# Optimization experiments

Hardware: AMD Instinct MI355X
Metric: run time of the kernel (lower is better)

Reference implementation:

```python
import jax, jax.numpy as jnp
import numpy as np

D_MODEL = 768
NUM_HEADS = 12
D_HEAD = D_MODEL // NUM_HEADS


def setup_inputs() -> dict:
    key = jax.random.key(0)
    ks = jax.random.split(key, 12)
    B, S = 2, 2048
    s = 1.0 / np.sqrt(D_MODEL)
    inp = {
        "query": jax.random.normal(ks[0], (B, S, D_MODEL), dtype=jnp.float32),
        "key": jax.random.normal(ks[1], (B, S, D_MODEL), dtype=jnp.float32),
        "value": jax.random.normal(ks[2], (B, S, D_MODEL), dtype=jnp.float32),
        "mask": jax.random.randint(ks[3], (B, 1, 1, S), 0, 2, dtype=jnp.int32),
        "Wq": jax.random.normal(ks[4], (D_MODEL, D_MODEL), dtype=jnp.float32) * s,
        "bq": jnp.zeros((D_MODEL,), dtype=jnp.float32),
        "Wk": jax.random.normal(ks[5], (D_MODEL, D_MODEL), dtype=jnp.float32) * s,
        "bk": jnp.zeros((D_MODEL,), dtype=jnp.float32),
        "Wv": jax.random.normal(ks[6], (D_MODEL, D_MODEL), dtype=jnp.float32) * s,
        "bv": jnp.zeros((D_MODEL,), dtype=jnp.float32),
        "Wo": jax.random.normal(ks[7], (D_MODEL, D_MODEL), dtype=jnp.float32) * s,
        "bo": jnp.zeros((D_MODEL,), dtype=jnp.float32),
    }
    return inp


def _split_heads(x):
    # [B, S, D] -> [B, H, S, Dh]
    B, S, _ = x.shape
    return x.reshape(B, S, NUM_HEADS, D_HEAD).transpose(0, 2, 1, 3)


def reference(query, key, value, mask, Wq, bq, Wk, bk, Wv, bv, Wo, bo):
    q = _split_heads(query @ Wq + bq)
    k = _split_heads(key @ Wk + bk)
    v = _split_heads(value @ Wv + bv)
    scores = jnp.einsum("bhqd,bhkd->bhqk", q, k) / jnp.sqrt(jnp.float32(D_HEAD))
    scores = jnp.where(mask == 0, -jnp.inf, scores)
    attn = jax.nn.softmax(scores, axis=-1)  # dropout is identity at inference
    ctx = jnp.einsum("bhqk,bhkd->bhqd", attn, v)
    B, _, S, _ = ctx.shape
    ctx = ctx.transpose(0, 2, 1, 3).reshape(B, S, D_MODEL)
    return ctx @ Wo + bo
```

## Files before the change

kernel.cpp:

```cpp
#include <hip/hip_runtime.h>
#include <stdint.h>

#define D_MODEL 768
#define SEQ     2048
#define BATCH   2
#define NHEAD   12
#define DHEAD   64
#define MROWS   (BATCH * SEQ)

typedef __bf16 bf16x8 __attribute__((ext_vector_type(8)));
typedef float  f32x4  __attribute__((ext_vector_type(4)));
typedef unsigned short u16;
typedef u16 u16x4 __attribute__((ext_vector_type(4)));
typedef uint32_t u32;

__device__ __forceinline__ u16 f32_to_bf16(float x) {
    u32 u = __float_as_uint(x);
    u32 r = (u + 0x7FFFu + ((u >> 16) & 1u)) >> 16;
    return (u16)r;
}
__device__ __forceinline__ float bf16_to_f32(u16 h) {
    return __uint_as_float(((u32)h) << 16);
}
__device__ __forceinline__ void split2(float x, u16 &hi, u16 &lo) {
    hi = f32_to_bf16(x);
    lo = f32_to_bf16(x - bf16_to_f32(hi));
}
__device__ __forceinline__ u32 pack2t(float a, float b) {
    return __builtin_amdgcn_perm(__float_as_uint(b), __float_as_uint(a), 0x07060302u);
}

__device__ __forceinline__ void stage16(const u16* g, const u16* l) {
    __builtin_amdgcn_global_load_lds(
        (const __attribute__((address_space(1))) u32*)g,
        (__attribute__((address_space(3))) u32*)l,
        16, 0, 0);
}

#define SRC_C8(lane)  ((((lane) & 3) ^ (((lane) >> 3) & 3)) * 8)
#define RD_C8(quad, l16) (((quad) ^ (((l16) >> 1) & 3)) * 8)

#define QSCALE 0.1803368801111204f
#define MSHIFT 20.0f

__global__ void prep_all(const float* __restrict__ q, const float* __restrict__ k,
                         const float* __restrict__ v, u16* __restrict__ xbase,
                         const float* __restrict__ Wq, const float* __restrict__ Wk,
                         const float* __restrict__ Wv, const float* __restrict__ Wo,
                         u16* __restrict__ wtbase,
                         const int* __restrict__ Mask, float* __restrict__ BiasM)
{
    __shared__ float tile[32][33];
    const int bx = blockIdx.x;
    if (bx < 9216) {
        const int t = bx / 3072;
        const float* src = (t == 0) ? q : (t == 1) ? k : v;
        const size_t P = (size_t)MROWS * D_MODEL;
        u16* xh = xbase + (size_t)t * 2 * P;
        u16* xl = xh + P;
        size_t idx = ((size_t)(bx % 3072) * 256 + threadIdx.x) * 4;
        float4 val = *reinterpret_cast<const float4*>(&src[idx]);
        float vv[4] = {val.x, val.y, val.z, val.w};
        u16x4 h4, l4;
        #pragma unroll
        for (int j = 0; j < 4; ++j) { u16 h, l; split2(vv[j], h, l); h4[j] = h; l4[j] = l; }
        *reinterpret_cast<u16x4*>(&xh[idx]) = h4;
        *reinterpret_cast<u16x4*>(&xl[idx]) = l4;
    } else if (bx < 11520) {
        int r = bx - 9216;
        int w = r / 576; r %= 576;
        int ky = r / 24, nx = r % 24;
        const float* W = (w == 0) ? Wq : (w == 1) ? Wk : (w == 2) ? Wv : Wo;
        const size_t WP = (size_t)D_MODEL * D_MODEL;
        u16* th = wtbase + (size_t)w * 2 * WP;
        u16* tl = th + WP;
        const int tx = threadIdx.x & 31, ty = threadIdx.x >> 5;
        const int n0 = nx * 32, k0 = ky * 32;
        #pragma unroll
        for (int rr = 0; rr < 4; ++rr) {
            int kk = k0 + ty + rr * 8;
            tile[ty + rr * 8][tx] = W[(size_t)kk * D_MODEL + n0 + tx];
        }
        __syncthreads();
        #pragma unroll
        for (int rr = 0; rr < 4; ++rr) {
            int n = n0 + ty + rr * 8;
            float val = tile[tx][ty + rr * 8];
            u16 h, l; split2(val, h, l);
            th[(size_t)n * D_MODEL + k0 + tx] = h;
            tl[(size_t)n * D_MODEL + k0 + tx] = l;
        }
    } else {
        int i = (bx - 11520) * 256 + threadIdx.x;
        BiasM[i] = (Mask[i] == 0) ? -3e38f : -MSHIFT;
    }
}

__global__ __launch_bounds__(256, 4) void gemm3(
    const u16* __restrict__ Ah0, const u16* __restrict__ Al0,
    const u16* __restrict__ Ah1, const u16* __restrict__ Al1,
    const u16* __restrict__ Ah2, const u16* __restrict__ Al2,
    const u16* __restrict__ Bh0, const u16* __restrict__ Bl0,
    const u16* __restrict__ Bh1, const u16* __restrict__ Bl1,
    const u16* __restrict__ Bh2, const u16* __restrict__ Bl2,
    const float* __restrict__ bias0, const float* __restrict__ bias1,
    const float* __restrict__ bias2,
    u16* __restrict__ Qhl, u16* __restrict__ Khl, u16* __restrict__ Vt,
    float* __restrict__ Out, int mode)
{
    const int z = (mode == 3) ? 3 : (int)blockIdx.z;
    const u16 *GAh, *GAl, *GBh, *GBl; const float* Bias;
    if (z == 1)      { GAh = Ah1; GAl = Al1; GBh = Bh1; GBl = Bl1; Bias = bias1; }
    else if (z == 2) { GAh = Ah2; GAl = Al2; GBh = Bh2; GBl = Bl2; Bias = bias2; }
    else             { GAh = Ah0; GAl = Al0; GBh = Bh0; GBl = Bl0; Bias = bias0; }

    const int m0 = blockIdx.x * 128;
    const int n0 = blockIdx.y * 64;
    const int tid  = threadIdx.x;
    const int wave = tid >> 6, lane = tid & 63;
    const int quad = lane >> 4, l16 = lane & 15;
    const int wm = wave & 1, wn = wave >> 1;

    __shared__ u16 sAh[128 * 32];
    __shared__ u16 sAl[128 * 32];
    __shared__ u16 sBh[64 * 32];
    __shared__ u16 sBl[64 * 32];

    const int srow = lane >> 2;
    const int sc8  = SRC_C8(lane);
    const int rc8  = RD_C8(quad, l16);

    f32x4 acc[4][2] = {};

    for (int k0 = 0; k0 < D_MODEL; k0 += 32) {
        {
            #pragma unroll
            for (int i = 0; i < 2; ++i) {
                int row = wave * 32 + i * 16 + srow;
                size_t ga = (size_t)(m0 + row) * D_MODEL + k0 + sc8;
                int ldst = (wave * 32 + i * 16) * 32;
                stage16(&GAh[ga], &sAh[ldst]);
                stage16(&GAl[ga], &sAl[ldst]);
            }
            int row = wave * 16 + srow;
            size_t gb = (size_t)(n0 + row) * D_MODEL + k0 + sc8;
            int ldst = (wave * 16) * 32;
            stage16(&GBh[gb], &sBh[ldst]);
            stage16(&GBl[gb], &sBl[ldst]);
        }
        asm volatile("s_waitcnt vmcnt(0)" ::: "memory");
        __syncthreads();

        bf16x8 afh[4], afl[4], bfh[2], bfl[2];
        #pragma unroll
        for (int t = 0; t < 4; ++t) {
            int ar = wm * 64 + t * 16 + l16;
            afh[t] = *reinterpret_cast<const bf16x8*>(&sAh[ar * 32 + rc8]);
            afl[t] = *reinterpret_cast<const bf16x8*>(&sAl[ar * 32 + rc8]);
        }
        #pragma unroll
        for (int t = 0; t < 2; ++t) {
            int bc = wn * 32 + t * 16 + l16;
            bfh[t] = *reinterpret_cast<const bf16x8*>(&sBh[bc * 32 + rc8]);
            bfl[t] = *reinterpret_cast<const bf16x8*>(&sBl[bc * 32 + rc8]);
        }
        #pragma unroll
        for (int mt = 0; mt < 4; ++mt) {
            #pragma unroll
            for (int nt = 0; nt < 2; ++nt) {
                f32x4 a = acc[mt][nt];
                a = __builtin_amdgcn_mfma_f32_16x16x32_bf16(afh[mt], bfh[nt], a, 0, 0, 0);
                a = __builtin_amdgcn_mfma_f32_16x16x32_bf16(afh[mt], bfl[nt], a, 0, 0, 0);
                a = __builtin_amdgcn_mfma_f32_16x16x32_bf16(afl[mt], bfh[nt], a, 0, 0, 0);
                acc[mt][nt] = a;
            }
        }
        __syncthreads();
    }

    #pragma unroll
    for (int nt = 0; nt < 2; ++nt) {
        int n = n0 + wn * 32 + nt * 16 + l16;
        float bv = Bias[n];
        #pragma unroll
        for (int mt = 0; mt < 4; ++mt) {
            #pragma unroll
            for (int r = 0; r < 4; ++r) {
                int m = m0 + wm * 64 + mt * 16 + quad * 4 + r;
                float v = acc[mt][nt][r] + bv;
                if (mode == 3) {
                    Out[(size_t)m * D_MODEL + n] = v;
                } else {
                    int b = m >> 11, s = m & (SEQ - 1);
                    int h = n >> 6, d = n & 63;
                    size_t bh = (size_t)(b * NHEAD + h);
                    if (z == 0) {
                        u16 hi, lo; split2(v * QSCALE, hi, lo);
                        u16* base = &Qhl[(bh * SEQ + s) * 128];
                        base[d] = hi; base[d + 64] = lo;
                    } else if (z == 1) {
                        u16 hi, lo; split2(v, hi, lo);
                        u16* base = &Khl[(bh * SEQ + s) * 128];
                        base[d] = hi; base[d + 64] = lo;
                    } else {
                        Vt[(bh * DHEAD + d) * SEQ + s] = f32_to_bf16(v);
                    }
                }
            }
        }
    }
}

__global__ __launch_bounds__(256, 3) void attn_kernel(
    const u16* __restrict__ Qhl, const u16* __restrict__ Khl, const u16* __restrict__ Vt,
    const float* __restrict__ BiasM, float* __restrict__ Opart,
    float* __restrict__ Lpart)
{
    const int qt   = blockIdx.x;
    const int bh   = blockIdx.y;
    const int half = blockIdx.z;
    const int b    = bh / NHEAD;
    const int tid  = threadIdx.x;
    const int wave = tid >> 6, lane = tid & 63;
    const int quad = lane >> 4, l16 = lane & 15;

    __shared__ u16 sK[4 * 2048];
    __shared__ u16 sV[2 * 2048];

    bf16x8 qh0[2], qh1[2], ql0[2], ql1[2];
    #pragma unroll
    for (int g = 0; g < 2; ++g) {
        const u16* qbase = &Qhl[((size_t)bh * SEQ + qt * 128 + wave * 32 + g * 16 + l16) * 128];
        qh0[g] = *reinterpret_cast<const bf16x8*>(&qbase[quad * 8]);
        qh1[g] = *reinterpret_cast<const bf16x8*>(&qbase[32 + quad * 8]);
        ql0[g] = *reinterpret_cast<const bf16x8*>(&qbase[64 + quad * 8]);
        ql1[g] = *reinterpret_cast<const bf16x8*>(&qbase[96 + quad * 8]);
    }

    union OU { u16 u[8]; bf16x8 v; } onesu;
    #pragma unroll
    for (int j = 0; j < 8; ++j) onesu.u[j] = 0x3F80;
    const bf16x8 ones = onesu.v;

    f32x4 oacc[2][4] = {};
    f32x4 lacc[2] = {};

    const float* biasb = &BiasM[b * SEQ];
    const int srcl0 = (((quad * 2) & 3) << 4) | l16;
    const int srcl1 = (((quad * 2 + 1) & 3) << 4) | l16;
    const bool selhi = (quad >> 1) != 0;

    const int strow = wave * 16 + (lane >> 2);
    const int stc8  = SRC_C8(lane);
    const int rc8   = RD_C8(quad, l16);
    const u16* kgb = &Khl[(size_t)bh * SEQ * 128];
    const u16* vgb = &Vt[(size_t)bh * DHEAD * SEQ];

    const int kvbeg = half * (SEQ / 2);
    for (int kv0 = kvbeg; kv0 < kvbeg + SEQ / 2; kv0 += 64) {
        #pragma unroll
        for (int j = 0; j < 4; ++j)
            stage16(&kgb[(size_t)(kv0 + strow) * 128 + j * 32 + stc8],
                    &sK[j * 2048 + wave * 512]);
        #pragma unroll
        for (int j = 0; j < 2; ++j)
            stage16(&vgb[(size_t)strow * SEQ + kv0 + j * 32 + stc8],
                    &sV[j * 2048 + wave * 512]);
        asm volatile("s_waitcnt vmcnt(0)" ::: "memory");
        __syncthreads();

        f32x4 binit[4];
        #pragma unroll
        for (int mt = 0; mt < 4; ++mt) {
            float4 b4 = *reinterpret_cast<const float4*>(
                &biasb[kv0 + mt * 16 + quad * 4]);
            binit[mt][0] = b4.x; binit[mt][1] = b4.y;
            binit[mt][2] = b4.z; binit[mt][3] = b4.w;
        }

        f32x4 sacc[2][4];
        #pragma unroll
        for (int mt = 0; mt < 4; ++mt) {
            const int rb = (mt * 16 + l16) * 32 + rc8;
            bf16x8 kh0 = *reinterpret_cast<const bf16x8*>(&sK[rb]);
            bf16x8 kh1 = *reinterpret_cast<const bf16x8*>(&sK[2048 + rb]);
            bf16x8 kl0 = *reinterpret_cast<const bf16x8*>(&sK[4096 + rb]);
            bf16x8 kl1 = *reinterpret_cast<const bf16x8*>(&sK[6144 + rb]);
            #pragma unroll
            for (int g = 0; g < 2; ++g) {
                f32x4 s = binit[mt];
                s = __builtin_amdgcn_mfma_f32_16x16x32_bf16(kh0, qh0[g], s, 0, 0, 0);
                s = __builtin_amdgcn_mfma_f32_16x16x32_bf16(kh1, qh1[g], s, 0, 0, 0);
                s = __builtin_amdgcn_mfma_f32_16x16x32_bf16(kh0, ql0[g], s, 0, 0, 0);
                s = __builtin_amdgcn_mfma_f32_16x16x32_bf16(kh1, ql1[g], s, 0, 0, 0);
                s = __builtin_amdgcn_mfma_f32_16x16x32_bf16(kl0, qh0[g], s, 0, 0, 0);
                s = __builtin_amdgcn_mfma_f32_16x16x32_bf16(kl1, qh1[g], s, 0, 0, 0);
                sacc[g][mt] = s;
            }
        }

        union FU { u32 u[4]; bf16x8 v; } fr[2][2];
        #pragma unroll
        for (int g = 0; g < 2; ++g) {
            u32 pLo[4], pHi[4];
            #pragma unroll
            for (int mt = 0; mt < 4; ++mt) {
                float p0 = exp2f(sacc[g][mt][0]);
                float p1 = exp2f(sacc[g][mt][1]);
                float p2 = exp2f(sacc[g][mt][2]);
                float p3 = exp2f(sacc[g][mt][3]);
                pLo[mt] = pack2t(p0, p1);
                pHi[mt] = pack2t(p2, p3);
            }
            #pragma unroll
            for (int f = 0; f < 2; ++f) {
                u32 a, bb;
                a  = (u32)__shfl((int)pLo[2 * f],     srcl0, 64);
                bb = (u32)__shfl((int)pLo[2 * f + 1], srcl0, 64);
                fr[g][f].u[0] = selhi ? bb : a;
                a  = (u32)__shfl((int)pHi[2 * f],     srcl0, 64);
                bb = (u32)__shfl((int)pHi[2 * f + 1], srcl0, 64);
                fr[g][f].u[1] = selhi ? bb : a;
                a  = (u32)__shfl((int)pLo[2 * f],     srcl1, 64);
                bb = (u32)__shfl((int)pLo[2 * f + 1], srcl1, 64);
                fr[g][f].u[2] = selhi ? bb : a;
                a  = (u32)__shfl((int)pHi[2 * f],     srcl1, 64);
                bb = (u32)__shfl((int)pHi[2 * f + 1], srcl1, 64);
                fr[g][f].u[3] = selhi ? bb : a;
            }
        }

        #pragma unroll
        for (int dt = 0; dt < 4; ++dt) {
            const int rb = (dt * 16 + l16) * 32 + rc8;
            bf16x8 vb0 = *reinterpret_cast<const bf16x8*>(&sV[rb]);
            bf16x8 vb1 = *reinterpret_cast<const bf16x8*>(&sV[2048 + rb]);
            #pragma unroll
            for (int g = 0; g < 2; ++g) {
                oacc[g][dt] = __builtin_amdgcn_mfma_f32_16x16x32_bf16(vb0, fr[g][0].v, oacc[g][dt], 0, 0, 0);
                oacc[g][dt] = __builtin_amdgcn_mfma_f32_16x16x32_bf16(vb1, fr[g][1].v, oacc[g][dt], 0, 0, 0);
            }
        }
        #pragma unroll
        for (int g = 0; g < 2; ++g) {
            lacc[g] = __builtin_amdgcn_mfma_f32_16x16x32_bf16(ones, fr[g][0].v, lacc[g], 0, 0, 0);
            lacc[g] = __builtin_amdgcn_mfma_f32_16x16x32_bf16(ones, fr[g][1].v, lacc[g], 0, 0, 0);
        }
        __syncthreads();
    }

    #pragma unroll
    for (int g = 0; g < 2; ++g) {
        size_t rowb = ((size_t)(half * (BATCH * NHEAD) + bh)) * SEQ
                    + qt * 128 + wave * 32 + g * 16 + l16;
        float* ob = &Opart[rowb * 64];
        #pragma unroll
        for (int dt = 0; dt < 4; ++dt)
            *reinterpret_cast<f32x4*>(&ob[dt * 16 + quad * 4]) = oacc[g][dt];
        if (quad == 0) Lpart[rowb] = lacc[g][0];
    }
}

__global__ void attn_combine(const float* __restrict__ Opart,
                             const float* __restrict__ Lpart,
                             u16* __restrict__ CTXh, u16* __restrict__ CTXl)
{
    const int NROW = BATCH * NHEAD * SEQ;
    int t = blockIdx.x * 256 + threadIdx.x;
    int row = t >> 4;
    int d0 = (t & 15) << 2;
    float inv = 1.f / (Lpart[row] + Lpart[NROW + row]);
    f32x4 O0 = *reinterpret_cast<const f32x4*>(&Opart[(size_t)row * 64 + d0]);
    f32x4 O1 = *reinterpret_cast<const f32x4*>(&Opart[((size_t)NROW + row) * 64 + d0]);
    int bh = row >> 11, q = row & (SEQ - 1);
    int b = bh / NHEAD, h = bh % NHEAD;
    size_t off = ((size_t)(b * SEQ + q)) * D_MODEL + h * DHEAD + d0;
    u16x4 h4, l4;
    #pragma unroll
    for (int j = 0; j < 4; ++j) {
        float val = (O0[j] + O1[j]) * inv;
        u16 hi, lo; split2(val, hi, lo);
        h4[j] = hi; l4[j] = lo;
    }
    *reinterpret_cast<u16x4*>(&CTXh[off]) = h4;
    *reinterpret_cast<u16x4*>(&CTXl[off]) = l4;
}

extern "C" void kernel_launch(void* const* d_in, const int* in_sizes, int n_in,
                              void* d_out, int out_size, void* d_ws, size_t ws_size,
                              hipStream_t stream)
{
    const float* query = (const float*)d_in[0];
    const float* key   = (const float*)d_in[1];
    const float* value = (const float*)d_in[2];
    const int*   mask  = (const int*)d_in[3];
    const float* Wq = (const float*)d_in[4];
    const float* bq = (const float*)d_in[5];
    const float* Wk = (const float*)d_in[6];
    const float* bk = (const float*)d_in[7];
    const float* Wv = (const float*)d_in[8];
    const float* bv = (const float*)d_in[9];
    const float* Wo = (const float*)d_in[10];
    const float* bo = (const float*)d_in[11];

    char* ws = (char*)d_ws;
    const size_t P2  = (size_t)MROWS * D_MODEL * 2;
    const size_t WP2 = (size_t)D_MODEL * D_MODEL * 2;

    u16* Xbase = (u16*)ws;
    u16* Xh_q = Xbase;                       u16* Xl_q = (u16*)((char*)Xh_q + P2);
    u16* Xh_k = (u16*)((char*)Xbase + 2*P2); u16* Xl_k = (u16*)((char*)Xh_k + P2);
    u16* Xh_v = (u16*)((char*)Xbase + 4*P2); u16* Xl_v = (u16*)((char*)Xh_v + P2);

    char* wtb = ws + 6 * P2;
    u16* Wh_q = (u16*)wtb;                   u16* Wl_q = (u16*)(wtb + WP2);
    u16* Wh_k = (u16*)(wtb + 2*WP2);         u16* Wl_k = (u16*)(wtb + 3*WP2);
    u16* Wh_v = (u16*)(wtb + 4*WP2);         u16* Wl_v = (u16*)(wtb + 5*WP2);
    u16* Wh_o = (u16*)(wtb + 6*WP2);         u16* Wl_o = (u16*)(wtb + 7*WP2);

    char* qb = wtb + 8 * WP2;
    const size_t QK_BYTES = (size_t)BATCH * NHEAD * SEQ * 128 * 2;
    u16* QhlBuf = (u16*)qb;
    u16* KhlBuf = (u16*)(qb + QK_BYTES);
    u16* VtBuf  = (u16*)(qb + 2 * QK_BYTES);

    char* tail = qb + 2 * QK_BYTES + QK_BYTES / 2;
    float* BiasM = (float*)tail;
    float* Lpart = (float*)(tail + 16384);

    float* Opart = (float*)Xh_k;
    u16* CTXh = Xh_q; u16* CTXl = Xl_q;

    float* out = (float*)d_out;
    dim3 blk(256, 1, 1);

    prep_all<<<dim3(11536), blk, 0, stream>>>(
        query, key, value, Xbase, Wq, Wk, Wv, Wo, (u16*)wtb, mask, BiasM);

    gemm3<<<dim3(32, 12, 3), blk, 0, stream>>>(
        Xh_q, Xl_q, Xh_k, Xl_k, Xh_v, Xl_v,
        Wh_q, Wl_q, Wh_k, Wl_k, Wh_v, Wl_v,
        bq, bk, bv, QhlBuf, KhlBuf, VtBuf, nullptr, 0);

    attn_kernel<<<dim3(16, 24, 2), blk, 0, stream>>>(
        QhlBuf, KhlBuf, VtBuf, BiasM, Opart, Lpart);

    attn_combine<<<dim3(3072), blk, 0, stream>>>(Opart, Lpart, CTXh, CTXl);

    gemm3<<<dim3(32, 12, 1), blk, 0, stream>>>(
        CTXh, CTXl, nullptr, nullptr, nullptr, nullptr,
        Wh_o, Wl_o, nullptr, nullptr, nullptr, nullptr,
        bo, nullptr, nullptr, nullptr, nullptr, nullptr, out, 3);
}
```

Baseline: 267.7 us.

## Double-buffer K/V tiles in attention and swizzle block order across XCDs

The attention kernel now keeps two LDS buffers for the K and V tiles. It issues the global-to-LDS staging for the next 64-key tile before computing on the current one, and drops the trailing barrier, so load latency overlaps with MFMA work. The launch grid is flattened to 1D and remapped so that blocks sharing a head and key-half are spread in a way meant to help L2 locality across the XCDs. The extra buffers double LDS use per block, which may lower occupancy relative to the launch bound of 3 blocks.

```diff
diff --git a/kernel.cpp b/kernel.cpp
--- a/kernel.cpp
+++ b/kernel.cpp
@@ -216,16 +216,19 @@
     const float* __restrict__ BiasM, float* __restrict__ Opart,
     float* __restrict__ Lpart)
 {
-    const int qt   = blockIdx.x;
-    const int bh   = blockIdx.y;
-    const int half = blockIdx.z;
+    const int flat = blockIdx.x;
+    const int wk   = (flat & 7) * 96 + (flat >> 3);
+    const int qt   = wk & 15;
+    const int grp  = wk >> 4;
+    const int bh   = grp % 24;
+    const int half = grp / 24;
     const int b    = bh / NHEAD;
     const int tid  = threadIdx.x;
     const int wave = tid >> 6, lane = tid & 63;
     const int quad = lane >> 4, l16 = lane & 15;
 
-    __shared__ u16 sK[4 * 2048];
-    __shared__ u16 sV[2 * 2048];
+    __shared__ u16 sK[2][4 * 2048];
+    __shared__ u16 sV[2][2 * 2048];
 
     bf16x8 qh0[2], qh1[2], ql0[2], ql1[2];
     #pragma unroll
@@ -257,17 +260,36 @@
     const u16* vgb = &Vt[(size_t)bh * DHEAD * SEQ];
 
     const int kvbeg = half * (SEQ / 2);
-    for (int kv0 = kvbeg; kv0 < kvbeg + SEQ / 2; kv0 += 64) {
-        #pragma unroll
-        for (int j = 0; j < 4; ++j)
-            stage16(&kgb[(size_t)(kv0 + strow) * 128 + j * 32 + stc8],
-                    &sK[j * 2048 + wave * 512]);
-        #pragma unroll
-        for (int j = 0; j < 2; ++j)
-            stage16(&vgb[(size_t)strow * SEQ + kv0 + j * 32 + stc8],
-                    &sV[j * 2048 + wave * 512]);
+
+    #pragma unroll
+    for (int j = 0; j < 4; ++j)
+        stage16(&kgb[(size_t)(kvbeg + strow) * 128 + j * 32 + stc8],
+                &sK[0][j * 2048 + wave * 512]);
+    #pragma unroll
+    for (int j = 0; j < 2; ++j)
+        stage16(&vgb[(size_t)strow * SEQ + kvbeg + j * 32 + stc8],
+                &sV[0][j * 2048 + wave * 512]);
+
+    for (int it = 0; it < 16; ++it) {
+        const int kv0 = kvbeg + it * 64;
         asm volatile("s_waitcnt vmcnt(0)" ::: "memory");
         __syncthreads();
+
+        if (it + 1 < 16) {
+            const int kvn = kv0 + 64;
+            u16* dK = sK[(it + 1) & 1];
+            u16* dV = sV[(it + 1) & 1];
+            #pragma unroll
+            for (int j = 0; j < 4; ++j)
+                stage16(&kgb[(size_t)(kvn + strow) * 128 + j * 32 + stc8],
+                        &dK[j * 2048 + wave * 512]);
+            #pragma unroll
+            for (int j = 0; j < 2; ++j)
+                stage16(&vgb[(size_t)strow * SEQ + kvn + j * 32 + stc8],
+                        &dV[j * 2048 + wave * 512]);
+        }
+        const u16* cK = sK[it & 1];
+        const u16* cV = sV[it & 1];
 
         f32x4 binit[4];
         #pragma unroll
@@ -282,10 +304,10 @@
         #pragma unroll
         for (int mt = 0; mt < 4; ++mt) {
             const int rb = (mt * 16 + l16) * 32 + rc8;
-            bf16x8 kh0 = *reinterpret_cast<const bf16x8*>(&sK[rb]);
-            bf16x8 kh1 = *reinterpret_cast<const bf16x8*>(&sK[2048 + rb]);
-            bf16x8 kl0 = *reinterpret_cast<const bf16x8*>(&sK[4096 + rb]);
-            bf16x8 kl1 = *reinterpret_cast<const bf16x8*>(&sK[6144 + rb]);
+            bf16x8 kh0 = *reinterpret_cast<const bf16x8*>(&cK[rb]);
+            bf16x8 kh1 = *reinterpret_cast<const bf16x8*>(&cK[2048 + rb]);
+            bf16x8 kl0 = *reinterpret_cast<const bf16x8*>(&cK[4096 + rb]);
+            bf16x8 kl1 = *reinterpret_cast<const bf16x8*>(&cK[6144 + rb]);
             #pragma unroll
             for (int g = 0; g < 2; ++g) {
                 f32x4 s = binit[mt];
@@ -333,8 +355,8 @@
         #pragma unroll
         for (int dt = 0; dt < 4; ++dt) {
             const int rb = (dt * 16 + l16) * 32 + rc8;
-            bf16x8 vb0 = *reinterpret_cast<const bf16x8*>(&sV[rb]);
-            bf16x8 vb1 = *reinterpret_cast<const bf16x8*>(&sV[2048 + rb]);
+            bf16x8 vb0 = *reinterpret_cast<const bf16x8*>(&cV[rb]);
+            bf16x8 vb1 = *reinterpret_cast<const bf16x8*>(&cV[2048 + rb]);
             #pragma unroll
             for (int g = 0; g < 2; ++g) {
                 oacc[g][dt] = __builtin_amdgcn_mfma_f32_16x16x32_bf16(vb0, fr[g][0].v, oacc[g][dt], 0, 0, 0);
@@ -346,7 +368,6 @@
             lacc[g] = __builtin_amdgcn_mfma_f32_16x16x32_bf16(ones, fr[g][0].v, lacc[g], 0, 0, 0);
             lacc[g] = __builtin_amdgcn_mfma_f32_16x16x32_bf16(ones, fr[g][1].v, lacc[g], 0, 0, 0);
         }
-        __syncthreads();
     }
 
     #pragma unroll
@@ -442,7 +463,7 @@
         Wh_q, Wl_q, Wh_k, Wl_k, Wh_v, Wl_v,
         bq, bk, bv, QhlBuf, KhlBuf, VtBuf, nullptr, 0);
 
-    attn_kernel<<<dim3(16, 24, 2), blk, 0, stream>>>(
+    attn_kernel<<<dim3(768), blk, 0, stream>>>(
         QhlBuf, KhlBuf, VtBuf, BiasM, Opart, Lpart);
 
     attn_combine<<<dim3(3072), blk, 0, stream>>>(Opart, Lpart, CTXh, CTXl);
```

After: 266.1 us. Within noise of the previous version (-0.6%).

## Halve attention query tile to 64 rows and remap grid for XCD locality

Applied to the files above, without the earlier changes.

The attention kernel now has each wave handle 16 query rows instead of 32, so a block covers 64 queries and the grid doubles to 1536 flat blocks. The launch bound is raised from 3 to 6 blocks per CU to exploit the lower register use. Block indices are permuted so consecutive blocks on the same XCD (flat & 7) work on the same head and split, aiming for better L2 reuse of K and V. The trade-off is that each K/V tile staged in LDS is now reused by half as many queries, which doubles global/LDS staging traffic per unit of compute.

```diff
diff --git a/kernel.cpp b/kernel.cpp
--- a/kernel.cpp
+++ b/kernel.cpp
@@ -211,14 +211,17 @@
     }
 }
 
-__global__ __launch_bounds__(256, 3) void attn_kernel(
+__global__ __launch_bounds__(256, 6) void attn_kernel(
     const u16* __restrict__ Qhl, const u16* __restrict__ Khl, const u16* __restrict__ Vt,
     const float* __restrict__ BiasM, float* __restrict__ Opart,
     float* __restrict__ Lpart)
 {
-    const int qt   = blockIdx.x;
-    const int bh   = blockIdx.y;
-    const int half = blockIdx.z;
+    const int flat = blockIdx.x;
+    const int wk   = (flat & 7) * 192 + (flat >> 3);
+    const int qt   = wk & 31;
+    const int grp  = wk >> 5;
+    const int bh   = grp % 24;
+    const int half = grp / 24;
     const int b    = bh / NHEAD;
     const int tid  = threadIdx.x;
     const int wave = tid >> 6, lane = tid & 63;
@@ -227,23 +230,19 @@
     __shared__ u16 sK[4 * 2048];
     __shared__ u16 sV[2 * 2048];
 
-    bf16x8 qh0[2], qh1[2], ql0[2], ql1[2];
-    #pragma unroll
-    for (int g = 0; g < 2; ++g) {
-        const u16* qbase = &Qhl[((size_t)bh * SEQ + qt * 128 + wave * 32 + g * 16 + l16) * 128];
-        qh0[g] = *reinterpret_cast<const bf16x8*>(&qbase[quad * 8]);
-        qh1[g] = *reinterpret_cast<const bf16x8*>(&qbase[32 + quad * 8]);
-        ql0[g] = *reinterpret_cast<const bf16x8*>(&qbase[64 + quad * 8]);
-        ql1[g] = *reinterpret_cast<const bf16x8*>(&qbase[96 + quad * 8]);
-    }
+    const u16* qbase = &Qhl[((size_t)bh * SEQ + qt * 64 + wave * 16 + l16) * 128];
+    const bf16x8 qh0 = *reinterpret_cast<const bf16x8*>(&qbase[quad * 8]);
+    const bf16x8 qh1 = *reinterpret_cast<const bf16x8*>(&qbase[32 + quad * 8]);
+    const bf16x8 ql0 = *reinterpret_cast<const bf16x8*>(&qbase[64 + quad * 8]);
+    const bf16x8 ql1 = *reinterpret_cast<const bf16x8*>(&qbase[96 + quad * 8]);
 
     union OU { u16 u[8]; bf16x8 v; } onesu;
     #pragma unroll
     for (int j = 0; j < 8; ++j) onesu.u[j] = 0x3F80;
     const bf16x8 ones = onesu.v;
 
-    f32x4 oacc[2][4] = {};
-    f32x4 lacc[2] = {};
+    f32x4 oacc[4] = {};
+    f32x4 lacc = {};
 
     const float* biasb = &BiasM[b * SEQ];
     const int srcl0 = (((quad * 2) & 3) << 4) | l16;
@@ -278,7 +277,7 @@
             binit[mt][2] = b4.z; binit[mt][3] = b4.w;
         }
 
-        f32x4 sacc[2][4];
+        f32x4 sacc[4];
         #pragma unroll
         for (int mt = 0; mt < 4; ++mt) {
             const int rb = (mt * 16 + l16) * 32 + rc8;
@@ -286,29 +285,25 @@
             bf16x8 kh1 = *reinterpret_cast<const bf16x8*>(&sK[2048 + rb]);
             bf16x8 kl0 = *reinterpret_cast<const bf16x8*>(&sK[4096 + rb]);
             bf16x8 kl1 = *reinterpret_cast<const bf16x8*>(&sK[6144 + rb]);
-            #pragma unroll
-            for (int g = 0; g < 2; ++g) {
-                f32x4 s = binit[mt];
-                s = __builtin_amdgcn_mfma_f32_16x16x32_bf16(kh0, qh0[g], s, 0, 0, 0);
-                s = __builtin_amdgcn_mfma_f32_16x16x32_bf16(kh1, qh1[g], s, 0, 0, 0);
-                s = __builtin_amdgcn_mfma_f32_16x16x32_bf16(kh0, ql0[g], s, 0, 0, 0);
-                s = __builtin_amdgcn_mfma_f32_16x16x32_bf16(kh1, ql1[g], s, 0, 0, 0);
-                s = __builtin_amdgcn_mfma_f32_16x16x32_bf16(kl0, qh0[g], s, 0, 0, 0);
-                s = __builtin_amdgcn_mfma_f32_16x16x32_bf16(kl1, qh1[g], s, 0, 0, 0);
-                sacc[g][mt] = s;
-            }
-        }
-
-        union FU { u32 u[4]; bf16x8 v; } fr[2][2];
-        #pragma unroll
-        for (int g = 0; g < 2; ++g) {
+            f32x4 s = binit[mt];
+            s = __builtin_amdgcn_mfma_f32_16x16x32_bf16(kh0, qh0, s, 0, 0, 0);
+            s = __builtin_amdgcn_mfma_f32_16x16x32_bf16(kh1, qh1, s, 0, 0, 0);
+            s = __builtin_amdgcn_mfma_f32_16x16x32_bf16(kh0, ql0, s, 0, 0, 0);
+            s = __builtin_amdgcn_mfma_f32_16x16x32_bf16(kh1, ql1, s, 0, 0, 0);
+            s = __builtin_amdgcn_mfma_f32_16x16x32_bf16(kl0, qh0, s, 0, 0, 0);
+            s = __builtin_amdgcn_mfma_f32_16x16x32_bf16(kl1, qh1, s, 0, 0, 0);
+            sacc[mt] = s;
+        }
+
+        union FU { u32 u[4]; bf16x8 v; } fr[2];
+        {
             u32 pLo[4], pHi[4];
             #pragma unroll
             for (int mt = 0; mt < 4; ++mt) {
-                float p0 = exp2f(sacc[g][mt][0]);
-                float p1 = exp2f(sacc[g][mt][1]);
-                float p2 = exp2f(sacc[g][mt][2]);
-                float p3 = exp2f(sacc[g][mt][3]);
+                float p0 = exp2f(sacc[mt][0]);
+                float p1 = exp2f(sacc[mt][1]);
+                float p2 = exp2f(sacc[mt][2]);
+                float p3 = exp2f(sacc[mt][3]);
                 pLo[mt] = pack2t(p0, p1);
                 pHi[mt] = pack2t(p2, p3);
             }
@@ -317,16 +312,16 @@
                 u32 a, bb;
                 a  = (u32)__shfl((int)pLo[2 * f],     srcl0, 64);
                 bb = (u32)__shfl((int)pLo[2 * f + 1], srcl0, 64);
-                fr[g][f].u[0] = selhi ? bb : a;
+                fr[f].u[0] = selhi ? bb : a;
                 a  = (u32)__shfl((int)pHi[2 * f],     srcl0, 64);
                 bb = (u32)__shfl((int)pHi[2 * f + 1], srcl0, 64);
-                fr[g][f].u[1] = selhi ? bb : a;
+                fr[f].u[1] = selhi ? bb : a;
                 a  = (u32)__shfl((int)pLo[2 * f],     srcl1, 64);
                 bb = (u32)__shfl((int)pLo[2 * f + 1], srcl1, 64);
-                fr[g][f].u[2] = selhi ? bb : a;
+                fr[f].u[2] = selhi ? bb : a;
                 a  = (u32)__shfl((int)pHi[2 * f],     srcl1, 64);
                 bb = (u32)__shfl((int)pHi[2 * f + 1], srcl1, 64);
-                fr[g][f].u[3] = selhi ? bb : a;
+                fr[f].u[3] = selhi ? bb : a;
             }
         }
 
@@ -335,29 +330,23 @@
             const int rb = (dt * 16 + l16) * 32 + rc8;
             bf16x8 vb0 = *reinterpret_cast<const bf16x8*>(&sV[rb]);
             bf16x8 vb1 = *reinterpret_cast<const bf16x8*>(&sV[2048 + rb]);
-            #pragma unroll
-            for (int g = 0; g < 2; ++g) {
-                oacc[g][dt] = __builtin_amdgcn_mfma_f32_16x16x32_bf16(vb0, fr[g][0].v, oacc[g][dt], 0, 0, 0);
-                oacc[g][dt] = __builtin_amdgcn_mfma_f32_16x16x32_bf16(vb1, fr[g][1].v, oacc[g][dt], 0, 0, 0);
-            }
-        }
-        #pragma unroll
-        for (int g = 0; g < 2; ++g) {
-            lacc[g] = __builtin_amdgcn_mfma_f32_16x16x32_bf16(ones, fr[g][0].v, lacc[g], 0, 0, 0);
-            lacc[g] = __builtin_amdgcn_mfma_f32_16x16x32_bf16(ones, fr[g][1].v, lacc[g], 0, 0, 0);
-        }
+            oacc[dt] = __builtin_amdgcn_mfma_f32_16x16x32_bf16(vb0, fr[0].v, oacc[dt], 0, 0, 0);
+            oacc[dt] = __builtin_amdgcn_mfma_f32_16x16x32_bf16(vb1, fr[1].v, oacc[dt], 0, 0, 0);
+        }
+        lacc = __builtin_amdgcn_mfma_f32_16x16x32_bf16(ones, fr[0].v, lacc, 0, 0, 0);
+        lacc = __builtin_amdgcn_mfma_f32_16x16x32_bf16(ones, fr[1].v, lacc, 0, 0, 0);
+
         __syncthreads();
     }
 
-    #pragma unroll
-    for (int g = 0; g < 2; ++g) {
+    {
         size_t rowb = ((size_t)(half * (BATCH * NHEAD) + bh)) * SEQ
-                    + qt * 128 + wave * 32 + g * 16 + l16;
+                    + qt * 64 + wave * 16 + l16;
         float* ob = &Opart[rowb * 64];
         #pragma unroll
         for (int dt = 0; dt < 4; ++dt)
-            *reinterpret_cast<f32x4*>(&ob[dt * 16 + quad * 4]) = oacc[g][dt];
-        if (quad == 0) Lpart[rowb] = lacc[g][0];
+            *reinterpret_cast<f32x4*>(&ob[dt * 16 + quad * 4]) = oacc[dt];
+        if (quad == 0) Lpart[rowb] = lacc[0];
     }
 }
 
@@ -442,7 +431,7 @@
         Wh_q, Wl_q, Wh_k, Wl_k, Wh_v, Wl_v,
         bq, bk, bv, QhlBuf, KhlBuf, VtBuf, nullptr, 0);
 
-    attn_kernel<<<dim3(16, 24, 2), blk, 0, stream>>>(
+    attn_kernel<<<dim3(1536), blk, 0, stream>>>(
         QhlBuf, KhlBuf, VtBuf, BiasM, Opart, Lpart);
 
     attn_combine<<<dim3(3072), blk, 0, stream>>>(Opart, Lpart, CTXh, CTXl);
```

After: 306.7 us. +14.6%, slower.
